# Kernel optimization log

Hardware: AMD Instinct MI355X
Metric: run time of the kernel (lower is better)

The kernel has to match this reference:

```python
import jax, jax.numpy as jnp
import numpy as np

N, LN, S, T = 50000, 64, 8, 4
E = 800000
MU = 0.9


def setup_inputs() -> dict:
    key = jax.random.key(0)
    ks = jax.random.split(key, 10)
    X_Node = jax.random.randint(ks[0], (E,), 0, N, dtype=jnp.int64) if jax.config.jax_enable_x64 else jax.random.randint(ks[0], (E,), 0, N).astype(jnp.int32)
    X_Neis = jax.random.randint(ks[1], (E,), 0, N).astype(X_Node.dtype)
    dg_list = jax.random.randint(ks[2], (E,), 1, 64).astype(jnp.float32)
    sc = 0.05
    W_emb = jax.random.normal(ks[3], (N, LN), jnp.float32) * sc
    Wxi = jax.random.normal(ks[4], (2 * LN, S * S), jnp.float32) * sc
    bxi = jnp.zeros((S * S,), jnp.float32)
    Wrou = jax.random.normal(ks[5], (LN, S), jnp.float32) * sc
    brou = jnp.zeros((S,), jnp.float32)
    Wout = jax.random.normal(ks[6], (LN + S, 3), jnp.float32) * sc
    bout = jnp.zeros((3,), jnp.float32)
    return {"X_Node": X_Node, "X_Neis": X_Neis, "dg_list": dg_list,
            "W_emb": W_emb, "Wxi": Wxi, "bxi": bxi,
            "Wrou": Wrou, "brou": brou, "Wout": Wout, "bout": bout}


def reference(X_Node, X_Neis, dg_list, W_emb, Wxi, bxi, Wrou, brou, Wout, bout):
    # Edge-wise feature gather: X = [emb[src] || emb[dst]]  -> [E, 2*LN]
    node_e = W_emb[X_Node]
    neis_e = W_emb[X_Neis]
    X = jnp.concatenate([node_e, neis_e], axis=1)
    # Hw precompute (loop-invariant): A [E,S,S], b [E,S]
    A = jnp.tanh(X @ Wxi + bxi).reshape(-1, S, S) * (MU / S) / dg_list[:, None, None]
    b = jnp.tanh(node_e @ Wrou + brou)

    states = jnp.zeros((N, S), dtype=W_emb.dtype)

    def step(states, _):
        H = states[X_Node]                      # gather [E, S]
        H = jnp.einsum('eij,ej->ei', A, H) + b  # per-edge small matvec
        # AggrSum's one-hot [V,E] matmul == scatter-add by X_Node
        new_states = jax.ops.segment_sum(H, X_Node, num_segments=N)
        return new_states, None

    states, _ = jax.lax.scan(step, states, None, length=T)
    logits = jnp.concatenate([W_emb, states], axis=1) @ Wout + bout
    return jax.nn.softmax(logits, axis=1)
```

## Files before the change

### kernel.cpp

```cpp
#include <hip/hip_runtime.h>
#include <hip/hip_fp16.h>
#include <math.h>

#define N_NODES 50000
#define LNDIM   64
#define E_EDGES 800000
#define MU_OVER_S 0.1125f
#define HPAD 16
#define NRANGE 8
#define RANGE_SZ ((N_NODES + NRANGE - 1) / NRANGE)
#define MAXDEG 48
#define BCAP 110000
#define PRE_TPB 256
#define PRE_TILES ((N_NODES + PRE_TPB - 1) / PRE_TPB)
#define LDS_STRIDE 257
#define BK_EPT 16
#define BK_EPB (256 * BK_EPT)
#define BK_NB ((E_EDGES + BK_EPB - 1) / BK_EPB)
#define LOG2E 1.4426950408889634f

typedef _Float16 h2 __attribute__((ext_vector_type(2)));
typedef __fp16   fp16x2 __attribute__((ext_vector_type(2)));

__device__ __forceinline__ h2 bits_h2(unsigned u) {
    union { unsigned x; h2 h; } c; c.x = u; return c.h;
}
__device__ __forceinline__ unsigned h2_bits(h2 h) {
    union { h2 h; unsigned x; } c; c.h = h; return c.x;
}
__device__ __forceinline__ unsigned h2_bits(fp16x2 h) {
    union { fp16x2 h; unsigned x; } c; c.h = h; return c.x;
}

__global__ __launch_bounds__(256) void zero_kernel(int4* __restrict__ p, int n4)
{
    int i = blockIdx.x * 256 + threadIdx.x;
    if (i < n4) p[i] = make_int4(0, 0, 0, 0);
}

__global__ __launch_bounds__(256, 4) void fused_kernel(
    const float* __restrict__ W_emb, const float* __restrict__ Wxi,
    const float* __restrict__ bxi,   const float* __restrict__ Wrou,
    const float* __restrict__ brou,
    const int* __restrict__ X_Node, const int* __restrict__ X_Neis,
    const float* __restrict__ dg_list,
    unsigned short* __restrict__ T1, unsigned short* __restrict__ U,
    float* __restrict__ Bv, int* __restrict__ bkt_cursor,
    uint2* __restrict__ pairs)
{
    __shared__ float ldsT[32 * LDS_STRIDE];
    __shared__ int scnt[4][NRANGE];
    __shared__ int wpref[4][NRANGE];
    __shared__ int gbase[NRANGE];

    int tid = threadIdx.x;

    if (blockIdx.x < BK_NB) {
        int lane = tid & 63;
        int wid  = tid >> 6;
        int wavebase = blockIdx.x * BK_EPB + wid * (BK_EPT * 64);

        unsigned nd[BK_EPT], py[BK_EPT];
        int wcnt[NRANGE];
        #pragma unroll
        for (int r = 0; r < NRANGE; ++r) wcnt[r] = 0;

        #pragma unroll
        for (int i = 0; i < BK_EPT; ++i) {
            int e  = wavebase + i * 64 + lane;
            bool ok = e < E_EDGES;
            int ec = ok ? e : (E_EDGES - 1);
            int node = X_Node[ec];
            unsigned nei = (unsigned)X_Neis[ec];
            float sc = MU_OVER_S / dg_list[ec];
            __half_raw hr = __half_raw(__float2half(sc));
            py[i] = nei | ((unsigned)hr.x << 16);
            int r = ok ? (node / RANGE_SZ) : NRANGE;
            nd[i] = (unsigned)node | ((unsigned)r << 24);
            #pragma unroll
            for (int rr = 0; rr < NRANGE; ++rr)
                wcnt[rr] += __popcll(__ballot(r == rr));
        }

        if (lane < NRANGE) scnt[wid][lane] = wcnt[lane];
        __syncthreads();
        if (tid < NRANGE) {
            int c0 = scnt[0][tid], c1 = scnt[1][tid], c2 = scnt[2][tid], c3 = scnt[3][tid];
            wpref[0][tid] = 0;
            wpref[1][tid] = c0;
            wpref[2][tid] = c0 + c1;
            wpref[3][tid] = c0 + c1 + c2;
            gbase[tid] = atomicAdd(&bkt_cursor[tid * HPAD], c0 + c1 + c2 + c3);
        }
        __syncthreads();

        int wb[NRANGE];
        #pragma unroll
        for (int r = 0; r < NRANGE; ++r) wb[r] = gbase[r] + wpref[wid][r];

        #pragma unroll
        for (int i = 0; i < BK_EPT; ++i) {
            int r = nd[i] >> 24;
            #pragma unroll
            for (int rr = 0; rr < NRANGE; ++rr) {
                unsigned long long m = __ballot(r == rr);
                if (r == rr) {
                    int rank = __popcll(m & ((1ULL << lane) - 1ULL));
                    int pos  = wb[rr] + rank;
                    if (pos < BCAP)
                        pairs[(size_t)rr * BCAP + pos] =
                            make_uint2(nd[i] & 0xFFFFFFu, py[i]);
                }
                wb[rr] += __popcll(m);
            }
        }
        return;
    }

    int pb   = blockIdx.x - BK_NB;
    int pass = pb / PRE_TILES;
    int tile = pb % PRE_TILES;
    int base = tile * PRE_TPB;
    int v    = base + tid;

    if (pass == 4) {
        float acc[8];
        #pragma unroll
        for (int j = 0; j < 8; ++j) acc[j] = brou[j];
        for (int kc = 0; kc < 2; ++kc) {
            __syncthreads();
            #pragma unroll
            for (int c = 0; c < 8; ++c) {
                int idx  = c * PRE_TPB + tid;
                int node = idx >> 3, part = idx & 7;
                int nn   = min(base + node, N_NODES - 1);
                float4 q = *(const float4*)(W_emb + (size_t)nn * 64 + kc * 32 + part * 4);
                ldsT[(part*4+0)*LDS_STRIDE + node] = q.x;
                ldsT[(part*4+1)*LDS_STRIDE + node] = q.y;
                ldsT[(part*4+2)*LDS_STRIDE + node] = q.z;
                ldsT[(part*4+3)*LDS_STRIDE + node] = q.w;
            }
            __syncthreads();
            for (int kk = 0; kk < 32; ++kk) {
                float ek = ldsT[kk * LDS_STRIDE + tid];
                const float* wr = Wrou + (kc*32 + kk) * 8;
                #pragma unroll
                for (int j = 0; j < 8; ++j) acc[j] = fmaf(ek, wr[j], acc[j]);
            }
        }
        if (v < N_NODES) {
            float4* dst = (float4*)(Bv + (size_t)v * 8);
            dst[0] = make_float4(tanhf(acc[0]), tanhf(acc[1]), tanhf(acc[2]), tanhf(acc[3]));
            dst[1] = make_float4(tanhf(acc[4]), tanhf(acc[5]), tanhf(acc[6]), tanhf(acc[7]));
        }
        return;
    }

    int is_u  = pass >> 1;
    int jbase = (pass & 1) * 32;
    const float* W = Wxi + (is_u ? 64 * 64 : 0) + jbase;
    float acc[32];
    if (is_u) {
        #pragma unroll
        for (int j = 0; j < 32; ++j) acc[j] = 0.f;
    } else {
        #pragma unroll
        for (int j = 0; j < 32; ++j) acc[j] = bxi[jbase + j];
    }
    for (int kc = 0; kc < 2; ++kc) {
        __syncthreads();
        #pragma unroll
        for (int c = 0; c < 8; ++c) {
            int idx  = c * PRE_TPB + tid;
            int node = idx >> 3, part = idx & 7;
            int nn   = min(base + node, N_NODES - 1);
            float4 q = *(const float4*)(W_emb + (size_t)nn * 64 + kc * 32 + part * 4);
            ldsT[(part*4+0)*LDS_STRIDE + node] = q.x;
            ldsT[(part*4+1)*LDS_STRIDE + node] = q.y;
            ldsT[(part*4+2)*LDS_STRIDE + node] = q.z;
            ldsT[(part*4+3)*LDS_STRIDE + node] = q.w;
        }
        __syncthreads();
        for (int kk = 0; kk < 32; ++kk) {
            float ek = ldsT[kk * LDS_STRIDE + tid];
            const float* wr = W + (kc*32 + kk) * 64;
            #pragma unroll
            for (int j = 0; j < 32; ++j) acc[j] = fmaf(ek, wr[j], acc[j]);
        }
    }
    if (v >= N_NODES) return;
    unsigned short* outp = is_u ? U : T1;
    uint4* dst = (uint4*)(outp + (size_t)v * 64 + jbase);
    #pragma unroll
    for (int t = 0; t < 4; ++t) {
        uint4 q;
        q.x = h2_bits(__builtin_amdgcn_cvt_pkrtz(acc[8*t+0], acc[8*t+1]));
        q.y = h2_bits(__builtin_amdgcn_cvt_pkrtz(acc[8*t+2], acc[8*t+3]));
        q.z = h2_bits(__builtin_amdgcn_cvt_pkrtz(acc[8*t+4], acc[8*t+5]));
        q.w = h2_bits(__builtin_amdgcn_cvt_pkrtz(acc[8*t+6], acc[8*t+7]));
        dst[t] = q;
    }
}

__global__ __launch_bounds__(256) void scatter2_kernel(
    const uint2* __restrict__ pairs, const int* __restrict__ bkt_cursor,
    int* __restrict__ cnt_arr, unsigned* __restrict__ pk_s)
{
    int r = blockIdx.x & (NRANGE - 1);
    int i = (blockIdx.x >> 3) * 256 + threadIdx.x;
    if (i >= bkt_cursor[r * HPAD]) return;
    uint2 p = pairs[(size_t)r * BCAP + i];
    int pos = atomicAdd(&cnt_arr[(size_t)p.x * HPAD], 1);
    if (pos < MAXDEG) pk_s[(size_t)p.x * MAXDEG + pos] = p.y;
}

__global__ __launch_bounds__(256, 4) void main_kernel(
    const float* __restrict__ W_emb, const float* __restrict__ Wout,
    const float* __restrict__ bout,
    const unsigned short* __restrict__ T1, const unsigned short* __restrict__ U,
    const float* __restrict__ Bv, const int* __restrict__ cnt_arr,
    const unsigned* __restrict__ pk_s, float* __restrict__ out)
{
    int lane = threadIdx.x & 63;
    int wid  = threadIdx.x >> 6;
    int v    = blockIdx.x * 4 + wid;
    if (v >= N_NODES) return;

    int cntv = min(cnt_arr[(size_t)v * HPAD], MAXDEG);
    unsigned pkl = (lane < MAXDEG) ? pk_s[(size_t)v * MAXDEG + lane] : 0u;
    unsigned pk  = (lane < cntv) ? pkl : 0u;
    unsigned tu  = (unsigned)T1[(size_t)v * 64 + lane];
    h2 t2 = bits_h2(tu | (tu << 16));

    const h2 c1 = { (_Float16)0.13333334f,  (_Float16)0.13333334f };
    const h2 c0 = { (_Float16)-0.33333334f, (_Float16)-0.33333334f };

    float m0 = 0.f, m1 = 0.f;

    for (int k0 = 0; k0 < cntv; k0 += 16) {
        unsigned q[16], uu[16];
        #pragma unroll
        for (int x = 0; x < 16; ++x) {
            q[x]  = (unsigned)__builtin_amdgcn_readlane((int)pk, k0 + x);
            uu[x] = (unsigned)U[(size_t)(q[x] & 0xFFFFu) * 64 + lane];
        }
        __builtin_amdgcn_sched_barrier(0);
        #pragma unroll
        for (int p = 0; p < 8; ++p) {
            unsigned sc2 = (q[2*p] >> 16) | (q[2*p+1] & 0xFFFF0000u);
            h2 x   = bits_h2(uu[2*p] | (uu[2*p+1] << 16)) + t2;
            h2 x2  = x * x;
            h2 a   = x2 * c1 + c0;
            h2 th  = (x * x2) * a + x;
            if (p & 1) m1 = __builtin_amdgcn_fdot2(th, bits_h2(sc2), m1, false);
            else       m0 = __builtin_amdgcn_fdot2(th, bits_h2(sc2), m0, false);
        }
    }
    float macc = m0 + m1;

    int   j   = lane & 7;
    int   i   = lane >> 3;
    float cnt = (float)cntv;
    float cj  = cnt * Bv[v * 8 + j];
    float ci  = __shfl(cj, i);
    float sj  = cj;

    #pragma unroll
    for (int step = 0; step < 3; ++step) {
        float p = macc * sj;
        p += __shfl_xor(p, 1);
        p += __shfl_xor(p, 2);
        p += __shfl_xor(p, 4);
        float snew = p + ci;
        sj = __shfl(snew, j * 8);
    }

    float emb = W_emb[(size_t)v * 64 + lane];
    float p0 = emb * Wout[lane * 3 + 0];
    float p1 = emb * Wout[lane * 3 + 1];
    float p2 = emb * Wout[lane * 3 + 2];
    if (lane < 8) {
        p0 = fmaf(sj, Wout[(64 + lane) * 3 + 0], p0);
        p1 = fmaf(sj, Wout[(64 + lane) * 3 + 1], p1);
        p2 = fmaf(sj, Wout[(64 + lane) * 3 + 2], p2);
    }
    #pragma unroll
    for (int m = 1; m < 64; m <<= 1) {
        p0 += __shfl_xor(p0, m);
        p1 += __shfl_xor(p1, m);
        p2 += __shfl_xor(p2, m);
    }
    float L0 = p0 + bout[0], L1 = p1 + bout[1], L2 = p2 + bout[2];
    float mx = fmaxf(L0, fmaxf(L1, L2));
    float e0 = __builtin_amdgcn_exp2f((L0 - mx) * LOG2E);
    float e1 = __builtin_amdgcn_exp2f((L1 - mx) * LOG2E);
    float e2 = __builtin_amdgcn_exp2f((L2 - mx) * LOG2E);
    float inv = __builtin_amdgcn_rcpf(e0 + e1 + e2);
    float rr = (lane == 0) ? e0 : (lane == 1 ? e1 : e2);
    if (lane < 3) out[v * 3 + lane] = rr * inv;
}

extern "C" void kernel_launch(void* const* d_in, const int* in_sizes, int n_in,
                              void* d_out, int out_size, void* d_ws, size_t ws_size,
                              hipStream_t stream)
{
    const int*   X_Node = (const int*)  d_in[0];
    const int*   X_Neis = (const int*)  d_in[1];
    const float* dg     = (const float*)d_in[2];
    const float* W_emb  = (const float*)d_in[3];
    const float* Wxi    = (const float*)d_in[4];
    const float* bxi    = (const float*)d_in[5];
    const float* Wrou   = (const float*)d_in[6];
    const float* brou   = (const float*)d_in[7];
    const float* Wout   = (const float*)d_in[8];
    const float* bout   = (const float*)d_in[9];
    float*       out    = (float*)d_out;

    char*  ws  = (char*)d_ws;
    size_t off = 0;
    auto alloc = [&](size_t bytes) -> void* {
        void* p = ws + off;
        off += (bytes + 255) & ~(size_t)255;
        return p;
    };
    unsigned short* T1       = (unsigned short*)alloc((size_t)N_NODES * 64 * 2);
    unsigned short* U        = (unsigned short*)alloc((size_t)N_NODES * 64 * 2);
    float*          Bv       = (float*)alloc((size_t)N_NODES * 8 * 4);
    int*            cnt_arr  = (int*)  alloc((size_t)N_NODES * HPAD * 4);
    int*            bkt_cur  = (int*)  alloc((size_t)NRANGE * HPAD * 4);
    uint2*          pairs    = (uint2*)alloc((size_t)NRANGE * BCAP * 8);
    unsigned*       pk_s     = (unsigned*)alloc(((size_t)N_NODES * MAXDEG + 64) * 4);

    const int NZ4 = (N_NODES * HPAD + NRANGE * HPAD) / 4;

    zero_kernel<<<(NZ4 + 255) / 256, 256, 0, stream>>>((int4*)cnt_arr, NZ4);
    fused_kernel<<<BK_NB + PRE_TILES * 5, 256, 0, stream>>>(
        W_emb, Wxi, bxi, Wrou, brou, X_Node, X_Neis, dg,
        T1, U, Bv, bkt_cur, pairs);
    scatter2_kernel<<<((BCAP + 255) / 256) * NRANGE, 256, 0, stream>>>(
        pairs, bkt_cur, cnt_arr, pk_s);
    main_kernel<<<(N_NODES + 3) / 4, 256, 0, stream>>>(
        W_emb, Wout, bout, T1, U, Bv, cnt_arr, pk_s, out);
}
```

Before: 103.0 us.

## Fold cnt zeroing into bucket pass, precompute emb·Wout, shrink block sizes

Moves zeroing of the per-node count array into the bucketing blocks of the fused kernel, leaving a tiny zero kernel only for the bucket cursors. It precomputes the embedding part of the output logits (W_emb·Wout) per node in the Wrou pass, so the main kernel no longer reads W_emb or does a 64-lane reduction. It also halves the block size of the fused kernel, pads the per-node neighbour list stride to 64 for aligned loads, and raises the main kernel's occupancy hint. The cost is an extra per-node EW buffer, more launched blocks, and zeroing now sharing time with edge bucketing.

```diff
diff --git a/kernel.cpp b/kernel.cpp
--- a/kernel.cpp
+++ b/kernel.cpp
@@ -10,12 +10,14 @@
 #define NRANGE 8
 #define RANGE_SZ ((N_NODES + NRANGE - 1) / NRANGE)
 #define MAXDEG 48
+#define PKSTRIDE 64
 #define BCAP 110000
-#define PRE_TPB 256
+#define PRE_TPB 128
 #define PRE_TILES ((N_NODES + PRE_TPB - 1) / PRE_TPB)
-#define LDS_STRIDE 257
+#define LDS_STRIDE 129
+#define BK_TPB 128
 #define BK_EPT 16
-#define BK_EPB (256 * BK_EPT)
+#define BK_EPB (BK_TPB * BK_EPT)
 #define BK_NB ((E_EDGES + BK_EPB - 1) / BK_EPB)
 #define LOG2E 1.4426950408889634f
 
@@ -32,30 +34,37 @@
     union { fp16x2 h; unsigned x; } c; c.h = h; return c.x;
 }
 
-__global__ __launch_bounds__(256) void zero_kernel(int4* __restrict__ p, int n4)
-{
-    int i = blockIdx.x * 256 + threadIdx.x;
+__global__ __launch_bounds__(64) void zero_kernel(int4* __restrict__ p, int n4)
+{
+    int i = threadIdx.x;
     if (i < n4) p[i] = make_int4(0, 0, 0, 0);
 }
 
-__global__ __launch_bounds__(256, 4) void fused_kernel(
+__global__ __launch_bounds__(128, 4) void fused_kernel(
     const float* __restrict__ W_emb, const float* __restrict__ Wxi,
     const float* __restrict__ bxi,   const float* __restrict__ Wrou,
-    const float* __restrict__ brou,
+    const float* __restrict__ brou,  const float* __restrict__ Wout,
     const int* __restrict__ X_Node, const int* __restrict__ X_Neis,
     const float* __restrict__ dg_list,
     unsigned short* __restrict__ T1, unsigned short* __restrict__ U,
-    float* __restrict__ Bv, int* __restrict__ bkt_cursor,
+    float* __restrict__ Bv, float* __restrict__ EW,
+    int* __restrict__ cnt_arr, int* __restrict__ bkt_cursor,
     uint2* __restrict__ pairs)
 {
     __shared__ float ldsT[32 * LDS_STRIDE];
-    __shared__ int scnt[4][NRANGE];
-    __shared__ int wpref[4][NRANGE];
+    __shared__ int scnt[2][NRANGE];
+    __shared__ int wpref[2][NRANGE];
     __shared__ int gbase[NRANGE];
 
     int tid = threadIdx.x;
 
     if (blockIdx.x < BK_NB) {
+        {
+            int4* cz = (int4*)cnt_arr;
+            for (int i = blockIdx.x * BK_TPB + tid; i < N_NODES * HPAD / 4;
+                 i += BK_NB * BK_TPB)
+                cz[i] = make_int4(0, 0, 0, 0);
+        }
         int lane = tid & 63;
         int wid  = tid >> 6;
         int wavebase = blockIdx.x * BK_EPB + wid * (BK_EPT * 64);
@@ -85,12 +94,10 @@
         if (lane < NRANGE) scnt[wid][lane] = wcnt[lane];
         __syncthreads();
         if (tid < NRANGE) {
-            int c0 = scnt[0][tid], c1 = scnt[1][tid], c2 = scnt[2][tid], c3 = scnt[3][tid];
+            int c0 = scnt[0][tid], c1 = scnt[1][tid];
             wpref[0][tid] = 0;
             wpref[1][tid] = c0;
-            wpref[2][tid] = c0 + c1;
-            wpref[3][tid] = c0 + c1 + c2;
-            gbase[tid] = atomicAdd(&bkt_cursor[tid * HPAD], c0 + c1 + c2 + c3);
+            gbase[tid] = atomicAdd(&bkt_cursor[tid * HPAD], c0 + c1);
         }
         __syncthreads();
 
@@ -124,7 +131,7 @@
     int v    = base + tid;
 
     if (pass == 4) {
-        float acc[8];
+        float acc[8], ew0 = 0.f, ew1 = 0.f, ew2 = 0.f;
         #pragma unroll
         for (int j = 0; j < 8; ++j) acc[j] = brou[j];
         for (int kc = 0; kc < 2; ++kc) {
@@ -146,12 +153,17 @@
                 const float* wr = Wrou + (kc*32 + kk) * 8;
                 #pragma unroll
                 for (int j = 0; j < 8; ++j) acc[j] = fmaf(ek, wr[j], acc[j]);
+                const float* wo = Wout + (kc*32 + kk) * 3;
+                ew0 = fmaf(ek, wo[0], ew0);
+                ew1 = fmaf(ek, wo[1], ew1);
+                ew2 = fmaf(ek, wo[2], ew2);
             }
         }
         if (v < N_NODES) {
             float4* dst = (float4*)(Bv + (size_t)v * 8);
             dst[0] = make_float4(tanhf(acc[0]), tanhf(acc[1]), tanhf(acc[2]), tanhf(acc[3]));
             dst[1] = make_float4(tanhf(acc[4]), tanhf(acc[5]), tanhf(acc[6]), tanhf(acc[7]));
+            *(float4*)(EW + (size_t)v * 4) = make_float4(ew0, ew1, ew2, 0.f);
         }
         return;
     }
@@ -211,15 +223,15 @@
     if (i >= bkt_cursor[r * HPAD]) return;
     uint2 p = pairs[(size_t)r * BCAP + i];
     int pos = atomicAdd(&cnt_arr[(size_t)p.x * HPAD], 1);
-    if (pos < MAXDEG) pk_s[(size_t)p.x * MAXDEG + pos] = p.y;
-}
-
-__global__ __launch_bounds__(256, 4) void main_kernel(
-    const float* __restrict__ W_emb, const float* __restrict__ Wout,
-    const float* __restrict__ bout,
+    if (pos < MAXDEG) pk_s[(size_t)p.x * PKSTRIDE + pos] = p.y;
+}
+
+__global__ __launch_bounds__(256, 6) void main_kernel(
+    const float* __restrict__ Wout, const float* __restrict__ bout,
     const unsigned short* __restrict__ T1, const unsigned short* __restrict__ U,
-    const float* __restrict__ Bv, const int* __restrict__ cnt_arr,
-    const unsigned* __restrict__ pk_s, float* __restrict__ out)
+    const float* __restrict__ Bv, const float* __restrict__ EW,
+    const int* __restrict__ cnt_arr, const unsigned* __restrict__ pk_s,
+    float* __restrict__ out)
 {
     int lane = threadIdx.x & 63;
     int wid  = threadIdx.x >> 6;
@@ -227,7 +239,7 @@
     if (v >= N_NODES) return;
 
     int cntv = min(cnt_arr[(size_t)v * HPAD], MAXDEG);
-    unsigned pkl = (lane < MAXDEG) ? pk_s[(size_t)v * MAXDEG + lane] : 0u;
+    unsigned pkl = (lane < MAXDEG) ? pk_s[(size_t)v * PKSTRIDE + lane] : 0u;
     unsigned pk  = (lane < cntv) ? pkl : 0u;
     unsigned tu  = (unsigned)T1[(size_t)v * 64 + lane];
     h2 t2 = bits_h2(tu | (tu << 16));
@@ -275,22 +287,19 @@
         sj = __shfl(snew, j * 8);
     }
 
-    float emb = W_emb[(size_t)v * 64 + lane];
-    float p0 = emb * Wout[lane * 3 + 0];
-    float p1 = emb * Wout[lane * 3 + 1];
-    float p2 = emb * Wout[lane * 3 + 2];
-    if (lane < 8) {
-        p0 = fmaf(sj, Wout[(64 + lane) * 3 + 0], p0);
-        p1 = fmaf(sj, Wout[(64 + lane) * 3 + 1], p1);
-        p2 = fmaf(sj, Wout[(64 + lane) * 3 + 2], p2);
-    }
+    float p0 = sj * Wout[(64 + j) * 3 + 0];
+    float p1 = sj * Wout[(64 + j) * 3 + 1];
+    float p2 = sj * Wout[(64 + j) * 3 + 2];
     #pragma unroll
-    for (int m = 1; m < 64; m <<= 1) {
+    for (int m = 1; m < 8; m <<= 1) {
         p0 += __shfl_xor(p0, m);
         p1 += __shfl_xor(p1, m);
         p2 += __shfl_xor(p2, m);
     }
-    float L0 = p0 + bout[0], L1 = p1 + bout[1], L2 = p2 + bout[2];
+    float4 ewv = *(const float4*)(EW + (size_t)v * 4);
+    float L0 = p0 + ewv.x + bout[0];
+    float L1 = p1 + ewv.y + bout[1];
+    float L2 = p2 + ewv.z + bout[2];
     float mx = fmaxf(L0, fmaxf(L1, L2));
     float e0 = __builtin_amdgcn_exp2f((L0 - mx) * LOG2E);
     float e1 = __builtin_amdgcn_exp2f((L1 - mx) * LOG2E);
@@ -326,19 +335,18 @@
     unsigned short* T1       = (unsigned short*)alloc((size_t)N_NODES * 64 * 2);
     unsigned short* U        = (unsigned short*)alloc((size_t)N_NODES * 64 * 2);
     float*          Bv       = (float*)alloc((size_t)N_NODES * 8 * 4);
+    float*          EW       = (float*)alloc((size_t)N_NODES * 4 * 4);
     int*            cnt_arr  = (int*)  alloc((size_t)N_NODES * HPAD * 4);
     int*            bkt_cur  = (int*)  alloc((size_t)NRANGE * HPAD * 4);
     uint2*          pairs    = (uint2*)alloc((size_t)NRANGE * BCAP * 8);
-    unsigned*       pk_s     = (unsigned*)alloc(((size_t)N_NODES * MAXDEG + 64) * 4);
-
-    const int NZ4 = (N_NODES * HPAD + NRANGE * HPAD) / 4;
-
-    zero_kernel<<<(NZ4 + 255) / 256, 256, 0, stream>>>((int4*)cnt_arr, NZ4);
-    fused_kernel<<<BK_NB + PRE_TILES * 5, 256, 0, stream>>>(
-        W_emb, Wxi, bxi, Wrou, brou, X_Node, X_Neis, dg,
-        T1, U, Bv, bkt_cur, pairs);
+    unsigned*       pk_s     = (unsigned*)alloc((size_t)N_NODES * PKSTRIDE * 4);
+
+    zero_kernel<<<1, 64, 0, stream>>>((int4*)bkt_cur, NRANGE * HPAD / 4);
+    fused_kernel<<<BK_NB + PRE_TILES * 5, 128, 0, stream>>>(
+        W_emb, Wxi, bxi, Wrou, brou, Wout, X_Node, X_Neis, dg,
+        T1, U, Bv, EW, cnt_arr, bkt_cur, pairs);
     scatter2_kernel<<<((BCAP + 255) / 256) * NRANGE, 256, 0, stream>>>(
         pairs, bkt_cur, cnt_arr, pk_s);
     main_kernel<<<(N_NODES + 3) / 4, 256, 0, stream>>>(
-        W_emb, Wout, bout, T1, U, Bv, cnt_arr, pk_s, out);
-}
+        Wout, bout, T1, U, Bv, EW, cnt_arr, pk_s, out);
+}
```

Measured after the change: 117.9 us. +14.5%, slower.
